# Kernel tuning notes

Measured on AMD Instinct MI355X. Metric: run time of the kernel, lower is better.

Reference implementation:

```python
import jax, jax.numpy as jnp
import numpy as np
import math

B, T, IN_DIM, HID = 64, 512, 1024, 1024
TAU_MEM = 20.0
ALPHA = math.exp(-1.0 / TAU_MEM)
THRESHOLD = 1.0


def setup_inputs() -> dict:
    key = jax.random.key(0)
    kx, kw, kb = jax.random.split(key, 3)
    s = 1.0 / math.sqrt(IN_DIM)  # torch Linear default init scale
    x = jax.random.normal(kx, (B, T, IN_DIM), dtype=jnp.float32)
    W = jax.random.uniform(kw, (HID, IN_DIM), minval=-s, maxval=s, dtype=jnp.float32)
    b = jax.random.uniform(kb, (HID,), minval=-s, maxval=s, dtype=jnp.float32)
    return {"x": x, "W": W, "b": b}


def reference(x, W, b):
    # Precompute the batched GEMM once: I[b,t,h] = fc(x[:,t])
    I = jnp.einsum("bti,hi->bth", x, W) + b  # [B,T,H]

    def step(mem, I_t):
        mem = ALPHA * mem + I_t                         # leaky integrate
        spike = (mem >= THRESHOLD).astype(mem.dtype)    # fire
        mem = mem * (1.0 - spike)                       # hard reset
        return mem, spike

    mem0 = jnp.zeros((x.shape[0], HID), dtype=x.dtype)
    mem_final, spikes_tbh = jax.lax.scan(step, mem0, jnp.swapaxes(I, 0, 1))
    spikes = jnp.swapaxes(spikes_tbh, 0, 1)  # [B,T,H]
    return spikes, mem_final
```

## Files before the change

### kernel.cpp

```cpp
#include <hip/hip_runtime.h>

#define B_    64
#define T_    512
#define KDIM  1024
#define HID_  1024

#define BM 64
#define BN 64
#define BK 32
#define LDA 36
#define NSL 256
#define SPC 32
#define BOFF 2304

#define ALPHA_F 0.95122942450071400909f

typedef float v4f __attribute__((ext_vector_type(4)));
typedef float v2f __attribute__((ext_vector_type(2)));

__global__ __launch_bounds__(256, 2) void snn_np_db(
    const float* __restrict__ x,
    const float* __restrict__ W,
    const float* __restrict__ bias,
    float* __restrict__ spikes,
    float* __restrict__ memf)
{
#pragma clang fp contract(off)
    __shared__ float smem[9280];
    float* const AB0 = smem;
    float* const AB1 = smem + 4608;
    float* const Ism = smem + 4608;
    float* const bsh = smem + 9216;

    const int tid = threadIdx.x;
    const int bb  = blockIdx.x;
    const int h0  = blockIdx.y * BN;

    const int tx = tid & 15;
    const int ty = tid >> 4;

    const int sr0 = tid >> 3;
    const int sr1 = 32 + sr0;
    const int sc  = (tid & 7) << 2;

    const float* xb = x + (size_t)bb * T_ * KDIM;
    const float* Wb = W + (size_t)h0 * KDIM;

    if (tid < BN) bsh[tid] = bias[h0 + tid];

    float mem = 0.0f;

    float4 pa0, pa1, pw0, pw1;
    pa0 = *(const float4*)&xb[(size_t)sr0 * KDIM + sc];
    pa1 = *(const float4*)&xb[(size_t)sr1 * KDIM + sc];
    pw0 = *(const float4*)&Wb[(size_t)sr0 * KDIM + sc];
    pw1 = *(const float4*)&Wb[(size_t)sr1 * KDIM + sc];
    *(float4*)&AB0[sr0 * LDA + sc]        = pa0;
    *(float4*)&AB0[sr1 * LDA + sc]        = pa1;
    *(float4*)&AB0[BOFF + sr0 * LDA + sc] = pw0;
    *(float4*)&AB0[BOFF + sr1 * LDA + sc] = pw1;
    pa0 = *(const float4*)&xb[(size_t)sr0 * KDIM + 32 + sc];
    pa1 = *(const float4*)&xb[(size_t)sr1 * KDIM + 32 + sc];
    pw0 = *(const float4*)&Wb[(size_t)sr0 * KDIM + 32 + sc];
    pw1 = *(const float4*)&Wb[(size_t)sr1 * KDIM + 32 + sc];
    __syncthreads();

    for (int c = 0; c < T_ / BM; ++c) {
        v2f p01[4][4], p23[4][4];
#pragma unroll
        for (int j = 0; j < 4; ++j)
#pragma unroll
            for (int i = 0; i < 4; ++i) {
                p01[j][i] = (v2f)(0.0f);
                p23[j][i] = (v2f)(0.0f);
            }

        for (int s = 0; s < SPC; ++s) {
            const int g = c * SPC + s;
            float* const cb = (g & 1) ? AB1 : AB0;
            float* const nb = (g & 1) ? AB0 : AB1;

            if (g + 1 < NSL) {
                *(float4*)&nb[sr0 * LDA + sc]        = pa0;
                *(float4*)&nb[sr1 * LDA + sc]        = pa1;
                *(float4*)&nb[BOFF + sr0 * LDA + sc] = pw0;
                *(float4*)&nb[BOFF + sr1 * LDA + sc] = pw1;
            }
            if (g + 2 < NSL) {
                const int gs  = g + 2;
                const int nt0 = (gs >> 5) * BM;
                const int nk  = (gs & 31) << 5;
                pa0 = *(const float4*)&xb[(size_t)(nt0 + sr0) * KDIM + nk + sc];
                pa1 = *(const float4*)&xb[(size_t)(nt0 + sr1) * KDIM + nk + sc];
                pw0 = *(const float4*)&Wb[(size_t)sr0 * KDIM + nk + sc];
                pw1 = *(const float4*)&Wb[(size_t)sr1 * KDIM + nk + sc];
            }
#pragma unroll
            for (int kb = 0; kb < 2; ++kb) {
#pragma unroll
                for (int q = 3; q >= 0; --q) {
                    const int qc = (kb << 4) + (q << 2);
                    v2f a01[4], a23[4], b01[4], b23[4];
#pragma unroll
                    for (int j = 0; j < 4; ++j) {
                        const v4f a = *(const v4f*)&cb[(ty + 16 * j) * LDA + qc];
                        a01[j] = a.xy; a23[j] = a.zw;
                    }
#pragma unroll
                    for (int i = 0; i < 4; ++i) {
                        const v4f b = *(const v4f*)&cb[BOFF + (tx + 16 * i) * LDA + qc];
                        b01[i] = b.xy; b23[i] = b.zw;
                    }
#pragma unroll
                    for (int j = 0; j < 4; ++j)
#pragma unroll
                        for (int i = 0; i < 4; ++i) {
                            const v2f m01 = a01[j] * b01[i];
                            const v2f m23 = a23[j] * b23[i];
                            p01[j][i] = p01[j][i] + m01;
                            p23[j][i] = p23[j][i] + m23;
                        }
                }
            }
            __syncthreads();
        }

#pragma unroll
        for (int j = 0; j < 4; ++j)
#pragma unroll
            for (int i = 0; i < 4; ++i) {
                const float s01 = p01[j][i].x + p01[j][i].y;
                const float s23 = p23[j][i].x + p23[j][i].y;
                Ism[(ty + 16 * j) * (BN + 1) + (tx + 16 * i)] =
                    (s01 + s23) + bsh[tx + 16 * i];
            }
        __syncthreads();

        if (tid < BN) {
            const size_t srow0 = ((size_t)(bb * T_ + c * BM)) * HID_ + h0 + tid;
#pragma unroll 4
            for (int t = 0; t < BM; ++t) {
                const float It = Ism[t * (BN + 1) + tid];
                const float am = ALPHA_F * mem;
                mem = am + It;
                const bool fire = (mem >= 1.0f);
                spikes[srow0 + (size_t)t * HID_] = fire ? 1.0f : 0.0f;
                if (fire) mem = 0.0f;
            }
        }
        __syncthreads();
    }

    if (tid < BN) memf[(size_t)bb * HID_ + h0 + tid] = mem;
}

extern "C" void kernel_launch(void* const* d_in, const int* in_sizes, int n_in,
                              void* d_out, int out_size, void* d_ws, size_t ws_size,
                              hipStream_t stream) {
    const float* x    = (const float*)d_in[0];
    const float* W    = (const float*)d_in[1];
    const float* bias = (const float*)d_in[2];
    float* out    = (float*)d_out;
    float* spikes = out;
    float* memf   = out + (size_t)B_ * T_ * HID_;

    dim3 grid(B_, HID_ / BN);
    snn_np_db<<<grid, dim3(256), 0, stream>>>(x, W, bias, spikes, memf);
}
```

Before: 1.505 ms.

## Widen hidden tile to 128 and split k-lanes across thread pairs

Doubles the hidden-dimension tile per block from 64 to 128, so each x tile loaded from global memory is reused across twice as many output columns and the grid halves. Each pair of threads now splits the four k-lanes of a column and combines partial sums with a lane shuffle before writing to shared memory, which keeps the original summation order. In exchange, the accumulator register footprint per thread doubles, shared memory use grows to about 61 KB per block, and fewer blocks are available to fill the GPU.

```diff
diff --git a/kernel.cpp b/kernel.cpp
--- a/kernel.cpp
+++ b/kernel.cpp
@@ -6,19 +6,22 @@
 #define HID_  1024
 
 #define BM 64
-#define BN 64
+#define BN 128
 #define BK 32
 #define LDA 36
 #define NSL 256
 #define SPC 32
 #define BOFF 2304
+#define BUFSZ 6912
+#define ISMOFF 6912
+#define ISMLD 129
+#define BSHOFF 15168
 
 #define ALPHA_F 0.95122942450071400909f
 
-typedef float v4f __attribute__((ext_vector_type(4)));
 typedef float v2f __attribute__((ext_vector_type(2)));
 
-__global__ __launch_bounds__(256, 2) void snn_np_db(
+__global__ __launch_bounds__(256, 2) void snn_np_pair(
     const float* __restrict__ x,
     const float* __restrict__ W,
     const float* __restrict__ bias,
@@ -26,22 +29,23 @@
     float* __restrict__ memf)
 {
 #pragma clang fp contract(off)
-    __shared__ float smem[9280];
+    __shared__ float smem[15296];
     float* const AB0 = smem;
-    float* const AB1 = smem + 4608;
-    float* const Ism = smem + 4608;
-    float* const bsh = smem + 9216;
+    float* const AB1 = smem + BUFSZ;
+    float* const Ism = smem + ISMOFF;
+    float* const bsh = smem + BSHOFF;
 
     const int tid = threadIdx.x;
     const int bb  = blockIdx.x;
     const int h0  = blockIdx.y * BN;
 
-    const int tx = tid & 15;
-    const int ty = tid >> 4;
+    const int sub = tid & 1;
+    const int p   = tid >> 1;
+    const int px  = p & 15;
+    const int pt  = p >> 4;
 
-    const int sr0 = tid >> 3;
-    const int sr1 = 32 + sr0;
-    const int sc  = (tid & 7) << 2;
+    const int srow = tid >> 3;
+    const int scol = (tid & 7) << 2;
 
     const float* xb = x + (size_t)bb * T_ * KDIM;
     const float* Wb = W + (size_t)h0 * KDIM;
@@ -50,30 +54,36 @@
 
     float mem = 0.0f;
 
-    float4 pa0, pa1, pw0, pw1;
-    pa0 = *(const float4*)&xb[(size_t)sr0 * KDIM + sc];
-    pa1 = *(const float4*)&xb[(size_t)sr1 * KDIM + sc];
-    pw0 = *(const float4*)&Wb[(size_t)sr0 * KDIM + sc];
-    pw1 = *(const float4*)&Wb[(size_t)sr1 * KDIM + sc];
-    *(float4*)&AB0[sr0 * LDA + sc]        = pa0;
-    *(float4*)&AB0[sr1 * LDA + sc]        = pa1;
-    *(float4*)&AB0[BOFF + sr0 * LDA + sc] = pw0;
-    *(float4*)&AB0[BOFF + sr1 * LDA + sc] = pw1;
-    pa0 = *(const float4*)&xb[(size_t)sr0 * KDIM + 32 + sc];
-    pa1 = *(const float4*)&xb[(size_t)sr1 * KDIM + 32 + sc];
-    pw0 = *(const float4*)&Wb[(size_t)sr0 * KDIM + 32 + sc];
-    pw1 = *(const float4*)&Wb[(size_t)sr1 * KDIM + 32 + sc];
+    float4 pa0, pa1, pw0, pw1, pw2, pw3;
+    pa0 = *(const float4*)&xb[(size_t)(srow)      * KDIM + scol];
+    pa1 = *(const float4*)&xb[(size_t)(32 + srow) * KDIM + scol];
+    pw0 = *(const float4*)&Wb[(size_t)(srow)      * KDIM + scol];
+    pw1 = *(const float4*)&Wb[(size_t)(32 + srow) * KDIM + scol];
+    pw2 = *(const float4*)&Wb[(size_t)(64 + srow) * KDIM + scol];
+    pw3 = *(const float4*)&Wb[(size_t)(96 + srow) * KDIM + scol];
+    *(float4*)&AB0[srow * LDA + scol]               = pa0;
+    *(float4*)&AB0[(32 + srow) * LDA + scol]        = pa1;
+    *(float4*)&AB0[BOFF + srow * LDA + scol]        = pw0;
+    *(float4*)&AB0[BOFF + (32 + srow) * LDA + scol] = pw1;
+    *(float4*)&AB0[BOFF + (64 + srow) * LDA + scol] = pw2;
+    *(float4*)&AB0[BOFF + (96 + srow) * LDA + scol] = pw3;
+    pa0 = *(const float4*)&xb[(size_t)(srow)      * KDIM + 32 + scol];
+    pa1 = *(const float4*)&xb[(size_t)(32 + srow) * KDIM + 32 + scol];
+    pw0 = *(const float4*)&Wb[(size_t)(srow)      * KDIM + 32 + scol];
+    pw1 = *(const float4*)&Wb[(size_t)(32 + srow) * KDIM + 32 + scol];
+    pw2 = *(const float4*)&Wb[(size_t)(64 + srow) * KDIM + 32 + scol];
+    pw3 = *(const float4*)&Wb[(size_t)(96 + srow) * KDIM + 32 + scol];
     __syncthreads();
 
+    const int aoff = pt * LDA + 2 * sub;
+    const int boff = BOFF + px * LDA + 2 * sub;
+
     for (int c = 0; c < T_ / BM; ++c) {
-        v2f p01[4][4], p23[4][4];
+        v2f acc[8][8];
 #pragma unroll
-        for (int j = 0; j < 4; ++j)
+        for (int j = 0; j < 8; ++j)
 #pragma unroll
-            for (int i = 0; i < 4; ++i) {
-                p01[j][i] = (v2f)(0.0f);
-                p23[j][i] = (v2f)(0.0f);
-            }
+            for (int i = 0; i < 8; ++i) acc[j][i] = (v2f)(0.0f);
 
         for (int s = 0; s < SPC; ++s) {
             const int g = c * SPC + s;
@@ -81,44 +91,42 @@
             float* const nb = (g & 1) ? AB0 : AB1;
 
             if (g + 1 < NSL) {
-                *(float4*)&nb[sr0 * LDA + sc]        = pa0;
-                *(float4*)&nb[sr1 * LDA + sc]        = pa1;
-                *(float4*)&nb[BOFF + sr0 * LDA + sc] = pw0;
-                *(float4*)&nb[BOFF + sr1 * LDA + sc] = pw1;
+                *(float4*)&nb[srow * LDA + scol]               = pa0;
+                *(float4*)&nb[(32 + srow) * LDA + scol]        = pa1;
+                *(float4*)&nb[BOFF + srow * LDA + scol]        = pw0;
+                *(float4*)&nb[BOFF + (32 + srow) * LDA + scol] = pw1;
+                *(float4*)&nb[BOFF + (64 + srow) * LDA + scol] = pw2;
+                *(float4*)&nb[BOFF + (96 + srow) * LDA + scol] = pw3;
             }
             if (g + 2 < NSL) {
                 const int gs  = g + 2;
                 const int nt0 = (gs >> 5) * BM;
                 const int nk  = (gs & 31) << 5;
-                pa0 = *(const float4*)&xb[(size_t)(nt0 + sr0) * KDIM + nk + sc];
-                pa1 = *(const float4*)&xb[(size_t)(nt0 + sr1) * KDIM + nk + sc];
-                pw0 = *(const float4*)&Wb[(size_t)sr0 * KDIM + nk + sc];
-                pw1 = *(const float4*)&Wb[(size_t)sr1 * KDIM + nk + sc];
+                pa0 = *(const float4*)&xb[(size_t)(nt0 + srow)      * KDIM + nk + scol];
+                pa1 = *(const float4*)&xb[(size_t)(nt0 + 32 + srow) * KDIM + nk + scol];
+                pw0 = *(const float4*)&Wb[(size_t)(srow)      * KDIM + nk + scol];
+                pw1 = *(const float4*)&Wb[(size_t)(32 + srow) * KDIM + nk + scol];
+                pw2 = *(const float4*)&Wb[(size_t)(64 + srow) * KDIM + nk + scol];
+                pw3 = *(const float4*)&Wb[(size_t)(96 + srow) * KDIM + nk + scol];
             }
 #pragma unroll
             for (int kb = 0; kb < 2; ++kb) {
 #pragma unroll
                 for (int q = 3; q >= 0; --q) {
                     const int qc = (kb << 4) + (q << 2);
-                    v2f a01[4], a23[4], b01[4], b23[4];
+                    v2f av[8], bv[8];
 #pragma unroll
-                    for (int j = 0; j < 4; ++j) {
-                        const v4f a = *(const v4f*)&cb[(ty + 16 * j) * LDA + qc];
-                        a01[j] = a.xy; a23[j] = a.zw;
-                    }
+                    for (int j = 0; j < 8; ++j)
+                        av[j] = *(const v2f*)&cb[aoff + j * (8 * LDA) + qc];
 #pragma unroll
-                    for (int i = 0; i < 4; ++i) {
-                        const v4f b = *(const v4f*)&cb[BOFF + (tx + 16 * i) * LDA + qc];
-                        b01[i] = b.xy; b23[i] = b.zw;
-                    }
+                    for (int i = 0; i < 8; ++i)
+                        bv[i] = *(const v2f*)&cb[boff + i * (16 * LDA) + qc];
 #pragma unroll
-                    for (int j = 0; j < 4; ++j)
+                    for (int j = 0; j < 8; ++j)
 #pragma unroll
-                        for (int i = 0; i < 4; ++i) {
-                            const v2f m01 = a01[j] * b01[i];
-                            const v2f m23 = a23[j] * b23[i];
-                            p01[j][i] = p01[j][i] + m01;
-                            p23[j][i] = p23[j][i] + m23;
+                        for (int i = 0; i < 8; ++i) {
+                            const v2f m = av[j] * bv[i];
+                            acc[j][i] = acc[j][i] + m;
                         }
                 }
             }
@@ -126,13 +134,14 @@
         }
 
 #pragma unroll
-        for (int j = 0; j < 4; ++j)
+        for (int j = 0; j < 8; ++j)
 #pragma unroll
-            for (int i = 0; i < 4; ++i) {
-                const float s01 = p01[j][i].x + p01[j][i].y;
-                const float s23 = p23[j][i].x + p23[j][i].y;
-                Ism[(ty + 16 * j) * (BN + 1) + (tx + 16 * i)] =
-                    (s01 + s23) + bsh[tx + 16 * i];
+            for (int i = 0; i < 8; ++i) {
+                const float sh = acc[j][i].x + acc[j][i].y;
+                const float so = __shfl_xor(sh, 1, 64);
+                if (sub == 0)
+                    Ism[(pt + 8 * j) * ISMLD + (px + 16 * i)] =
+                        (sh + so) + bsh[px + 16 * i];
             }
         __syncthreads();
 
@@ -140,7 +149,7 @@
             const size_t srow0 = ((size_t)(bb * T_ + c * BM)) * HID_ + h0 + tid;
 #pragma unroll 4
             for (int t = 0; t < BM; ++t) {
-                const float It = Ism[t * (BN + 1) + tid];
+                const float It = Ism[t * ISMLD + tid];
                 const float am = ALPHA_F * mem;
                 mem = am + It;
                 const bool fire = (mem >= 1.0f);
@@ -165,5 +174,5 @@
     float* memf   = out + (size_t)B_ * T_ * HID_;
 
     dim3 grid(B_, HID_ / BN);
-    snn_np_db<<<grid, dim3(256), 0, stream>>>(x, W, bias, spikes, memf);
+    snn_np_pair<<<grid, dim3(256), 0, stream>>>(x, W, bias, spikes, memf);
 }
```

After: 1.589 ms. 1.06x slower.
